# Performance work log

Hardware: AMD Instinct MI355X
Metric: run time of the kernel (lower is better)

Reference implementation:

```python
import jax, jax.numpy as jnp
import numpy as np

S, B, E2 = 128, 32, 1024   # src_len, batch, 2*encoder_hidden
DH = 512                   # decoder_hidden
AH = 32                    # attn_hidden
EMB = 256                  # embedding_dim
V = 32000                  # output_dim (vocab)


def setup_inputs() -> dict:
    key = jax.random.key(0)
    ks = jax.random.split(key, 14)
    sc = 0.02
    inp = {
        "encoder_output": jax.random.normal(ks[0], (S, B, E2), jnp.float32),
        "max_length": 48,
        "sos_token": 1,
        "emb": jax.random.normal(ks[1], (V, EMB), jnp.float32) * sc,
        "W1": jax.random.normal(ks[2], (AH, DH + E2), jnp.float32) * sc,
        "b1": jnp.zeros((AH,), jnp.float32),
        "W2": jax.random.normal(ks[3], (1, AH), jnp.float32) * sc,
        "b2": jnp.zeros((1,), jnp.float32),
        "W_ih": jax.random.normal(ks[4], (3 * DH, E2 + EMB), jnp.float32) * sc,
        "b_ih": jnp.zeros((3 * DH,), jnp.float32),
        "W_hh": jax.random.normal(ks[5], (3 * DH, DH), jnp.float32) * sc,
        "b_hh": jnp.zeros((3 * DH,), jnp.float32),
        "Wo": jax.random.normal(ks[6], (V, DH), jnp.float32) * sc,
        "bo": jnp.zeros((V,), jnp.float32),
    }
    return inp


def reference(encoder_output, max_length, sos_token, emb, W1, b1, W2, b2,
              W_ih, b_ih, W_hh, b_hh, Wo, bo):
    s, b, _ = encoder_output.shape
    dh = W_hh.shape[1]

    def step(carry, _):
        h, x_emb = carry                       # h: [B,DH], x_emb: [B,EMB]
        # Bahdanau-style attention: concat(hidden, enc) -> MLP -> softmax over S
        ai = jnp.concatenate(
            [jnp.broadcast_to(h[None], (s, b, dh)), encoder_output], axis=2)
        scores = jnp.maximum(ai @ W1.T + b1, 0.0) @ W2.T + b2   # [S,B,1]
        attn = jax.nn.softmax(scores[..., 0], axis=0)           # [S,B]
        context = jnp.einsum('sbe,sb->be', encoder_output, attn)  # [B,2E]
        # single-step GRU cell (torch gate order: r, z, n)
        x = jnp.concatenate([context, x_emb], axis=1)
        gi = x @ W_ih.T + b_ih
        gh = h @ W_hh.T + b_hh
        r = jax.nn.sigmoid(gi[:, :dh] + gh[:, :dh])
        z = jax.nn.sigmoid(gi[:, dh:2 * dh] + gh[:, dh:2 * dh])
        n = jnp.tanh(gi[:, 2 * dh:] + r * gh[:, 2 * dh:])
        h_new = (1.0 - z) * n + z * h
        logits = h_new @ Wo.T + bo                              # [B,V]
        ids = jnp.argmax(logits, axis=1)
        return (h_new, emb[ids]), logits

    h0 = jnp.zeros((b, dh), encoder_output.dtype)
    x0 = jnp.broadcast_to(emb[sos_token][None], (b, emb.shape[1]))
    _, out = jax.lax.scan(step, (h0, x0), None, length=max_length)
    return out  # [max_length, B, V]
```

## Files before the change

### kernel.cpp

```cpp
#include <hip/hip_runtime.h>
#include <hip/hip_bf16.h>
#include <math.h>

typedef __bf16 bf16x8 __attribute__((ext_vector_type(8)));
typedef __bf16 bf16x4 __attribute__((ext_vector_type(4)));
typedef float f32x4 __attribute__((ext_vector_type(4)));

#define S_LEN 128
#define BATCH 32
#define E2C 1024
#define DH 512
#define AH 32
#define EMBD 256
#define VOC 32000
#define TMAX 48
#define LCHN 250

#define MFMA16(a, b, c) __builtin_amdgcn_mfma_f32_16x16x32_bf16((a), (b), (c), 0, 0, 0)

#define OFF_HF0   0
#define OFF_HH0   65536
#define OFF_HL0   98304
#define OFF_HF1   131072
#define OFF_HH1   196608
#define OFF_HL1   229376
#define OFF_XH    262144
#define OFF_XL    344064
#define OFF_ENCW1 425984
#define OFF_PVAL  950272
#define OFF_PIDX  983040
#define OFF_WOH   1015808
#define OFF_WOL   33783808
#define OFF_WIHH  66551808
#define OFF_WIHL  70483968
#define OFF_WHHH  74416128
#define OFF_WHHL  75988992
#define WS_REQ    77561856ULL

__device__ __forceinline__ void split8(const float* __restrict__ p,
                                       bf16x8& hi, bf16x8& lo) {
  const f32x4 v0 = *(const f32x4*)p;
  const f32x4 v1 = *(const f32x4*)(p + 4);
  float t[8] = {v0[0], v0[1], v0[2], v0[3], v1[0], v1[1], v1[2], v1[3]};
  #pragma unroll
  for (int i = 0; i < 8; i++) {
    const __bf16 h = (__bf16)t[i];
    hi[i] = h;
    lo[i] = (__bf16)(t[i] - (float)h);
  }
}

__global__ __launch_bounds__(256) void k_init(unsigned int* __restrict__ p) {
  p[blockIdx.x * 256 + threadIdx.x] = 0u;
}

__global__ __launch_bounds__(256) void k_encw1(const float* __restrict__ enc,
                                               const float* __restrict__ W1,
                                               float* __restrict__ encW1) {
  __shared__ float el[E2C];
  __shared__ float red[256];
  const int tid = threadIdx.x;
  const int blk = blockIdx.x;
  for (int i = 0; i < 4; i++)
    el[tid + i * 256] = enc[(size_t)blk * E2C + tid + i * 256];
  __syncthreads();
  const int j = tid >> 3, c = tid & 7;
  const float* wrow = W1 + (size_t)j * (DH + E2C) + DH;
  float p = 0.f;
  for (int k = c * 128; k < c * 128 + 128; k++) p += el[k] * wrow[k];
  red[tid] = p;
  __syncthreads();
  if (c < 4) red[tid] += red[tid + 4];
  __syncthreads();
  if (c < 2) red[tid] += red[tid + 2];
  __syncthreads();
  if (c == 0) encW1[(size_t)blk * AH + j] = red[tid] + red[tid + 1];
}

__global__ __launch_bounds__(256) void k_split4(const float* __restrict__ src,
                                                __bf16* __restrict__ dh,
                                                __bf16* __restrict__ dl, int n4) {
  const int i = blockIdx.x * 256 + threadIdx.x;
  if (i >= n4) return;
  const f32x4 v = ((const f32x4*)src)[i];
  bf16x4 h4, l4;
  #pragma unroll
  for (int j = 0; j < 4; j++) {
    const float x = v[j];
    const __bf16 h = (__bf16)x;
    h4[j] = h;
    l4[j] = (__bf16)(x - (float)h);
  }
  *(bf16x4*)(dh + (size_t)i * 4) = h4;
  *(bf16x4*)(dl + (size_t)i * 4) = l4;
}

__global__ __launch_bounds__(256) void k_attn(int t,
    const float* __restrict__ enc, const int* __restrict__ sos,
    const float* __restrict__ emb,
    const float* __restrict__ W1, const float* __restrict__ b1,
    const float* __restrict__ W2, const float* __restrict__ b2,
    const float* __restrict__ encW1,
    const float* __restrict__ hf,
    const float* __restrict__ pval, const int* __restrict__ pidx,
    __bf16* __restrict__ xh, __bf16* __restrict__ xl) {
  __shared__ float hs[DH];
  __shared__ float hw[AH];
  __shared__ float sc[S_LEN];
  __shared__ float red[256];
  __shared__ int ri[256];
  __shared__ int s_id;
  const int tid = threadIdx.x;
  const int b = blockIdx.x >> 2;
  const int part = blockIdx.x & 3;

  if (part == 0) {
    if (t == 0) {
      if (tid == 0) s_id = sos[0];
    } else {
      if (tid < LCHN) { red[tid] = pval[b * 256 + tid]; ri[tid] = pidx[b * 256 + tid]; }
      else            { red[tid] = -INFINITY;           ri[tid] = 0x7fffffff; }
      __syncthreads();
      for (int off = 128; off >= 1; off >>= 1) {
        if (tid < off) {
          const float ov = red[tid + off]; const int oi = ri[tid + off];
          if (ov > red[tid] || (ov == red[tid] && oi < ri[tid])) { red[tid] = ov; ri[tid] = oi; }
        }
        __syncthreads();
      }
      if (tid == 0) s_id = ri[0];
    }
    __syncthreads();
    int id = s_id;
    if (id < 0 || id >= VOC) id = 0;
    const float e = emb[(size_t)id * EMBD + tid];
    const __bf16 eh = (__bf16)e;
    xh[b * 1280 + 1024 + tid] = eh;
    xl[b * 1280 + 1024 + tid] = (__bf16)(e - (float)eh);
  }

  hs[tid] = hf[b * DH + tid];
  hs[tid + 256] = hf[b * DH + tid + 256];
  __syncthreads();
  {
    const int j = tid >> 3, c = tid & 7;
    const float* wrow = W1 + (size_t)j * (DH + E2C);
    float p = 0.f;
    for (int k = c * 64; k < c * 64 + 64; k++) p += hs[k] * wrow[k];
    red[tid] = p;
  }
  __syncthreads();
  if ((tid & 7) < 4) red[tid] += red[tid + 4];
  __syncthreads();
  if ((tid & 7) < 2) red[tid] += red[tid + 2];
  __syncthreads();
  if ((tid & 7) == 0) hw[tid >> 3] = red[tid] + red[tid + 1] + b1[tid >> 3];
  __syncthreads();

  float ex = 0.f;
  if (tid < S_LEN) {
    const float* ew = encW1 + ((size_t)tid * BATCH + b) * AH;
    float sum = b2[0];
    #pragma unroll
    for (int j = 0; j < AH; j++) {
      const float v = ew[j] + hw[j];
      sum += fmaxf(v, 0.f) * W2[j];
    }
    sc[tid] = sum;
  }
  __syncthreads();
  if (tid < 128) red[tid] = sc[tid];
  __syncthreads();
  for (int off = 64; off >= 1; off >>= 1) {
    if (tid < off) red[tid] = fmaxf(red[tid], red[tid + off]);
    __syncthreads();
  }
  const float mx = red[0];
  __syncthreads();
  if (tid < 128) { ex = expf(sc[tid] - mx); red[tid] = ex; }
  __syncthreads();
  for (int off = 64; off >= 1; off >>= 1) {
    if (tid < off) red[tid] += red[tid + off];
    __syncthreads();
  }
  const float ssum = red[0];
  if (tid < 128) sc[tid] = ex / ssum;
  __syncthreads();

  const int e0 = part * 256 + tid;
  float aa = 0.f;
  for (int s = 0; s < S_LEN; s++)
    aa += sc[s] * enc[((size_t)s * BATCH + b) * E2C + e0];
  const __bf16 ch = (__bf16)aa;
  xh[b * 1280 + e0] = ch;
  xl[b * 1280 + e0] = (__bf16)(aa - (float)ch);
}

template<bool PRE>
__global__ __launch_bounds__(256) void k_gru(
    const __bf16* __restrict__ xh, const __bf16* __restrict__ xl,
    const float* __restrict__ Wih, const float* __restrict__ bih,
    const float* __restrict__ Whh, const float* __restrict__ bhh,
    const __bf16* __restrict__ Wihh, const __bf16* __restrict__ Wihl,
    const __bf16* __restrict__ Whhh, const __bf16* __restrict__ Whhl,
    const float* __restrict__ hf_in, const __bf16* __restrict__ hh_in,
    const __bf16* __restrict__ hl_in,
    float* __restrict__ hf_out, __bf16* __restrict__ hh_out,
    __bf16* __restrict__ hl_out) {
  __shared__ float lds[4][8][256];
  const int tid = threadIdx.x;
  const int wv = tid >> 6;
  const int lane = tid & 63;
  const int q = lane >> 4;
  const int ln = lane & 15;
  const int d = blockIdx.x * 16 + ln;

  f32x4 acc[4][2];
  const f32x4 z4 = {0.f, 0.f, 0.f, 0.f};
  #pragma unroll
  for (int t = 0; t < 4; t++) { acc[t][0] = z4; acc[t][1] = z4; }

  #pragma unroll
  for (int i = 0; i < 14; i++) {
    const int kk = wv * 32 + i * 128;
    const int ka = kk + q * 8;
    bf16x8 ah0, al0, ah1, al1;
    if (i < 10) {
      ah0 = *(const bf16x8*)(xh + ln * 1280 + ka);
      ah1 = *(const bf16x8*)(xh + (16 + ln) * 1280 + ka);
      al0 = *(const bf16x8*)(xl + ln * 1280 + ka);
      al1 = *(const bf16x8*)(xl + (16 + ln) * 1280 + ka);
    } else {
      const int kb = ka - 1280;
      ah0 = *(const bf16x8*)(hh_in + ln * 512 + kb);
      ah1 = *(const bf16x8*)(hh_in + (16 + ln) * 512 + kb);
      al0 = *(const bf16x8*)(hl_in + ln * 512 + kb);
      al1 = *(const bf16x8*)(hl_in + (16 + ln) * 512 + kb);
    }
    #pragma unroll
    for (int g = 0; g < 3; g++) {
      bf16x8 bh, bl;
      if (PRE) {
        if (i < 10) {
          bh = *(const bf16x8*)(Wihh + (size_t)(g * 512 + d) * 1280 + ka);
          bl = *(const bf16x8*)(Wihl + (size_t)(g * 512 + d) * 1280 + ka);
        } else {
          bh = *(const bf16x8*)(Whhh + (size_t)(g * 512 + d) * 512 + (ka - 1280));
          bl = *(const bf16x8*)(Whhl + (size_t)(g * 512 + d) * 512 + (ka - 1280));
        }
      } else {
        if (i < 10) split8(Wih + (size_t)(g * 512 + d) * 1280 + ka, bh, bl);
        else        split8(Whh + (size_t)(g * 512 + d) * 512 + (ka - 1280), bh, bl);
      }
      const int t = (g < 2) ? g : ((i < 10) ? 2 : 3);
      acc[t][0] = MFMA16(ah0, bh, acc[t][0]);
      acc[t][0] = MFMA16(al0, bh, acc[t][0]);
      acc[t][0] = MFMA16(ah0, bl, acc[t][0]);
      acc[t][1] = MFMA16(ah1, bh, acc[t][1]);
      acc[t][1] = MFMA16(al1, bh, acc[t][1]);
      acc[t][1] = MFMA16(ah1, bl, acc[t][1]);
    }
  }

  #pragma unroll
  for (int t = 0; t < 4; t++)
    #pragma unroll
    for (int mt = 0; mt < 2; mt++)
      #pragma unroll
      for (int r = 0; r < 4; r++)
        lds[wv][t * 2 + mt][(q * 4 + r) * 16 + ln] = acc[t][mt][r];
  __syncthreads();
  for (int idx = tid; idx < 8 * 256; idx += 256) {
    const int tt = idx >> 8, e = idx & 255;
    lds[0][tt][e] += lds[1][tt][e] + lds[2][tt][e] + lds[3][tt][e];
  }
  __syncthreads();

  for (int u = tid; u < 512; u += 256) {
    const int b = u >> 4, dd = u & 15;
    const int mt = b >> 4;
    const int e = (b & 15) * 16 + dd;
    const int dg = blockIdx.x * 16 + dd;
    const float rp  = lds[0][0 * 2 + mt][e] + bih[dg]        + bhh[dg];
    const float zp  = lds[0][1 * 2 + mt][e] + bih[DH + dg]   + bhh[DH + dg];
    const float gin = lds[0][2 * 2 + mt][e] + bih[2 * DH + dg];
    const float ghn = lds[0][3 * 2 + mt][e] + bhh[2 * DH + dg];
    const float rg = 1.f / (1.f + expf(-rp));
    const float zg = 1.f / (1.f + expf(-zp));
    const float ng = tanhf(gin + rg * ghn);
    const float hp = hf_in[b * DH + dg];
    const float hn = (1.f - zg) * ng + zg * hp;
    hf_out[b * DH + dg] = hn;
    const __bf16 hi = (__bf16)hn;
    hh_out[b * DH + dg] = hi;
    hl_out[b * DH + dg] = (__bf16)(hn - (float)hi);
  }
}

template<bool PRE>
__global__ __launch_bounds__(256) void k_logits(
    const __bf16* __restrict__ hh, const __bf16* __restrict__ hl,
    const float* __restrict__ Wo, const float* __restrict__ bo,
    const __bf16* __restrict__ Woh, const __bf16* __restrict__ Wol,
    float* __restrict__ outp, float* __restrict__ pval, int* __restrict__ pidx) {
  const int tid = threadIdx.x;
  const int w = tid >> 6;
  const int lane = tid & 63;
  const int quad = lane >> 4;
  const int ln = lane & 15;
  const int v0 = blockIdx.x * 128;

  f32x4 acc[2][2];
  const f32x4 z4 = {0.f, 0.f, 0.f, 0.f};
  #pragma unroll
  for (int m = 0; m < 2; m++)
    #pragma unroll
    for (int n = 0; n < 2; n++) acc[m][n] = z4;

  #pragma unroll 2
  for (int kk = 0; kk < 512; kk += 32) {
    const int ka = kk + quad * 8;
    const bf16x8 fh0 = *(const bf16x8*)(hh + ln * 512 + ka);
    const bf16x8 fh1 = *(const bf16x8*)(hh + (16 + ln) * 512 + ka);
    const bf16x8 fl0 = *(const bf16x8*)(hl + ln * 512 + ka);
    const bf16x8 fl1 = *(const bf16x8*)(hl + (16 + ln) * 512 + ka);
    #pragma unroll
    for (int nt = 0; nt < 2; nt++) {
      const int vr = v0 + (w * 2 + nt) * 16 + ln;
      bf16x8 bh, bl;
      if (PRE) {
        bh = *(const bf16x8*)(Woh + (size_t)vr * 512 + ka);
        bl = *(const bf16x8*)(Wol + (size_t)vr * 512 + ka);
      } else {
        split8(Wo + (size_t)vr * 512 + ka, bh, bl);
      }
      acc[0][nt] = MFMA16(fh0, bh, acc[0][nt]);
      acc[0][nt] = MFMA16(fl0, bh, acc[0][nt]);
      acc[0][nt] = MFMA16(fh0, bl, acc[0][nt]);
      acc[1][nt] = MFMA16(fh1, bh, acc[1][nt]);
      acc[1][nt] = MFMA16(fl1, bh, acc[1][nt]);
      acc[1][nt] = MFMA16(fh1, bl, acc[1][nt]);
    }
  }

  float bv[2][4]; int bi[2][4];
  #pragma unroll
  for (int m = 0; m < 2; m++)
    #pragma unroll
    for (int r = 0; r < 4; r++) { bv[m][r] = -INFINITY; bi[m][r] = 0x7fffffff; }

  #pragma unroll
  for (int nt = 0; nt < 2; nt++) {
    const int v = v0 + (w * 2 + nt) * 16 + ln;
    const float bias = bo[v];
    #pragma unroll
    for (int mt = 0; mt < 2; mt++) {
      #pragma unroll
      for (int r = 0; r < 4; r++) {
        const float val = acc[mt][nt][r] + bias;
        const int b = mt * 16 + quad * 4 + r;
        __builtin_nontemporal_store(val, &outp[(size_t)b * VOC + v]);
        if (val > bv[mt][r]) { bv[mt][r] = val; bi[mt][r] = v; }
      }
    }
  }
  #pragma unroll
  for (int m = 1; m < 16; m <<= 1) {
    #pragma unroll
    for (int mt = 0; mt < 2; mt++) {
      #pragma unroll
      for (int r = 0; r < 4; r++) {
        const float ov = __shfl_xor(bv[mt][r], m, 64);
        const int oi = __shfl_xor(bi[mt][r], m, 64);
        if (ov > bv[mt][r] || (ov == bv[mt][r] && oi < bi[mt][r])) {
          bv[mt][r] = ov; bi[mt][r] = oi;
        }
      }
    }
  }
  __shared__ float lv[128];
  __shared__ int li[128];
  if (ln == 0) {
    #pragma unroll
    for (int mt = 0; mt < 2; mt++)
      for (int r = 0; r < 4; r++) {
        const int b = mt * 16 + quad * 4 + r;
        lv[w * 32 + b] = bv[mt][r];
        li[w * 32 + b] = bi[mt][r];
      }
  }
  __syncthreads();
  if (tid < 32) {
    float bbv = lv[tid]; int bbi = li[tid];
    for (int w2 = 1; w2 < 4; w2++) {
      const float ov = lv[w2 * 32 + tid]; const int oi = li[w2 * 32 + tid];
      if (ov > bbv || (ov == bbv && oi < bbi)) { bbv = ov; bbi = oi; }
    }
    pval[tid * 256 + blockIdx.x] = bbv;
    pidx[tid * 256 + blockIdx.x] = bbi;
  }
}

extern "C" void kernel_launch(void* const* d_in, const int* in_sizes, int n_in,
                              void* d_out, int out_size, void* d_ws, size_t ws_size,
                              hipStream_t stream) {
  const float* enc = (const float*)d_in[0];
  const int* sos = (const int*)d_in[2];
  const float* emb = (const float*)d_in[3];
  const float* W1 = (const float*)d_in[4];
  const float* b1 = (const float*)d_in[5];
  const float* W2 = (const float*)d_in[6];
  const float* b2 = (const float*)d_in[7];
  const float* Wih = (const float*)d_in[8];
  const float* bih = (const float*)d_in[9];
  const float* Whh = (const float*)d_in[10];
  const float* bhh = (const float*)d_in[11];
  const float* Wo = (const float*)d_in[12];
  const float* bo = (const float*)d_in[13];

  char* ws = (char*)d_ws;
  float* hf[2]  = {(float*)(ws + OFF_HF0),  (float*)(ws + OFF_HF1)};
  __bf16* hh[2] = {(__bf16*)(ws + OFF_HH0), (__bf16*)(ws + OFF_HH1)};
  __bf16* hl[2] = {(__bf16*)(ws + OFF_HL0), (__bf16*)(ws + OFF_HL1)};
  __bf16* xh = (__bf16*)(ws + OFF_XH);
  __bf16* xl = (__bf16*)(ws + OFF_XL);
  float* encW1 = (float*)(ws + OFF_ENCW1);
  float* pval = (float*)(ws + OFF_PVAL);
  int* pidx = (int*)(ws + OFF_PIDX);
  __bf16* Woh  = (__bf16*)(ws + OFF_WOH);
  __bf16* Wol  = (__bf16*)(ws + OFF_WOL);
  __bf16* Wihh = (__bf16*)(ws + OFF_WIHH);
  __bf16* Wihl = (__bf16*)(ws + OFF_WIHL);
  __bf16* Whhh = (__bf16*)(ws + OFF_WHHH);
  __bf16* Whhl = (__bf16*)(ws + OFF_WHHL);

  k_init<<<128, 256, 0, stream>>>((unsigned int*)ws);
  k_encw1<<<S_LEN * BATCH, 256, 0, stream>>>(enc, W1, encW1);

  float* out = (float*)d_out;
  const bool pre = (ws_size >= WS_REQ);
  if (pre) {
    k_split4<<<16000, 256, 0, stream>>>(Wo,  Woh,  Wol,  4096000);
    k_split4<<<1920,  256, 0, stream>>>(Wih, Wihh, Wihl, 491520);
    k_split4<<<768,   256, 0, stream>>>(Whh, Whhh, Whhl, 196608);
  }

  for (int t = 0; t < TMAX; t++) {
    const int p = t & 1;
    k_attn<<<128, 256, 0, stream>>>(t, enc, sos, emb, W1, b1, W2, b2,
                                    encW1, hf[p], pval, pidx, xh, xl);
    if (pre) {
      k_gru<true><<<32, 256, 0, stream>>>(xh, xl, Wih, bih, Whh, bhh,
                                          Wihh, Wihl, Whhh, Whhl,
                                          hf[p], hh[p], hl[p],
                                          hf[p ^ 1], hh[p ^ 1], hl[p ^ 1]);
      k_logits<true><<<LCHN, 256, 0, stream>>>(hh[p ^ 1], hl[p ^ 1], Wo, bo, Woh, Wol,
                                               out + (size_t)t * BATCH * VOC, pval, pidx);
    } else {
      k_gru<false><<<32, 256, 0, stream>>>(xh, xl, Wih, bih, Whh, bhh,
                                           Wihh, Wihl, Whhh, Whhl,
                                           hf[p], hh[p], hl[p],
                                           hf[p ^ 1], hh[p ^ 1], hl[p ^ 1]);
      k_logits<false><<<LCHN, 256, 0, stream>>>(hh[p ^ 1], hl[p ^ 1], Wo, bo, Woh, Wol,
                                                out + (size_t)t * BATCH * VOC, pval, pidx);
    }
  }
}
```

Measured before the change: 3.079 ms.

## Fuse attention context into logits kernel and move argmax/embedding into GRU

Removes the per-step attention kernel. The context computation for the next step now runs as extra blocks appended to the logits launch, and a one-off context kernel covers step zero. The argmax reduction and embedding lookup move into the GRU kernel, which splits the embedding row to bf16 on the fly. The logits kernel goes to 512 threads with one 16-column tile per wave. The goal is one fewer launch and dependency point per decode step, at the cost of redundant argmax work in every GRU block.

Measured after the change: 3.341 ms. 8.5% more time.

```diff
diff --git a/kernel.cpp b/kernel.cpp
--- a/kernel.cpp
+++ b/kernel.cpp
@@ -15,6 +15,7 @@
 #define VOC 32000
 #define TMAX 48
 #define LCHN 250
+#define CTXB 64
 
 #define MFMA16(a, b, c) __builtin_amdgcn_mfma_f32_16x16x32_bf16((a), (b), (c), 0, 0, 0)
 
@@ -95,54 +96,22 @@
   *(bf16x4*)(dl + (size_t)i * 4) = l4;
 }
 
-__global__ __launch_bounds__(256) void k_attn(int t,
-    const float* __restrict__ enc, const int* __restrict__ sos,
-    const float* __restrict__ emb,
+__device__ __forceinline__ void ctx_block(int bc, int tid,
+    const float* __restrict__ enc,
     const float* __restrict__ W1, const float* __restrict__ b1,
     const float* __restrict__ W2, const float* __restrict__ b2,
-    const float* __restrict__ encW1,
-    const float* __restrict__ hf,
-    const float* __restrict__ pval, const int* __restrict__ pidx,
-    __bf16* __restrict__ xh, __bf16* __restrict__ xl) {
-  __shared__ float hs[DH];
-  __shared__ float hw[AH];
-  __shared__ float sc[S_LEN];
-  __shared__ float red[256];
-  __shared__ int ri[256];
-  __shared__ int s_id;
-  const int tid = threadIdx.x;
-  const int b = blockIdx.x >> 2;
-  const int part = blockIdx.x & 3;
-
-  if (part == 0) {
-    if (t == 0) {
-      if (tid == 0) s_id = sos[0];
-    } else {
-      if (tid < LCHN) { red[tid] = pval[b * 256 + tid]; ri[tid] = pidx[b * 256 + tid]; }
-      else            { red[tid] = -INFINITY;           ri[tid] = 0x7fffffff; }
-      __syncthreads();
-      for (int off = 128; off >= 1; off >>= 1) {
-        if (tid < off) {
-          const float ov = red[tid + off]; const int oi = ri[tid + off];
-          if (ov > red[tid] || (ov == red[tid] && oi < ri[tid])) { red[tid] = ov; ri[tid] = oi; }
-        }
-        __syncthreads();
-      }
-      if (tid == 0) s_id = ri[0];
-    }
-    __syncthreads();
-    int id = s_id;
-    if (id < 0 || id >= VOC) id = 0;
-    const float e = emb[(size_t)id * EMBD + tid];
-    const __bf16 eh = (__bf16)e;
-    xh[b * 1280 + 1024 + tid] = eh;
-    xl[b * 1280 + 1024 + tid] = (__bf16)(e - (float)eh);
-  }
-
-  hs[tid] = hf[b * DH + tid];
-  hs[tid + 256] = hf[b * DH + tid + 256];
-  __syncthreads();
-  {
+    const float* __restrict__ encW1, const float* __restrict__ hf,
+    __bf16* __restrict__ xh, __bf16* __restrict__ xl,
+    float* hs, float* hw, float* sc, float* red) {
+  const int b = bc >> 1;
+  const int part = bc & 1;
+
+  if (tid < 256) {
+    hs[tid] = hf[b * DH + tid];
+    hs[tid + 256] = hf[b * DH + tid + 256];
+  }
+  __syncthreads();
+  if (tid < 256) {
     const int j = tid >> 3, c = tid & 7;
     const float* wrow = W1 + (size_t)j * (DH + E2C);
     float p = 0.f;
@@ -150,11 +119,11 @@
     red[tid] = p;
   }
   __syncthreads();
-  if ((tid & 7) < 4) red[tid] += red[tid + 4];
-  __syncthreads();
-  if ((tid & 7) < 2) red[tid] += red[tid + 2];
-  __syncthreads();
-  if ((tid & 7) == 0) hw[tid >> 3] = red[tid] + red[tid + 1] + b1[tid >> 3];
+  if (tid < 256 && (tid & 7) < 4) red[tid] += red[tid + 4];
+  __syncthreads();
+  if (tid < 256 && (tid & 7) < 2) red[tid] += red[tid + 2];
+  __syncthreads();
+  if (tid < 256 && (tid & 7) == 0) hw[tid >> 3] = red[tid] + red[tid + 1] + b1[tid >> 3];
   __syncthreads();
 
   float ex = 0.f;
@@ -187,17 +156,33 @@
   if (tid < 128) sc[tid] = ex / ssum;
   __syncthreads();
 
-  const int e0 = part * 256 + tid;
+  const int e0 = part * 512 + tid;
   float aa = 0.f;
   for (int s = 0; s < S_LEN; s++)
     aa += sc[s] * enc[((size_t)s * BATCH + b) * E2C + e0];
   const __bf16 ch = (__bf16)aa;
-  xh[b * 1280 + e0] = ch;
-  xl[b * 1280 + e0] = (__bf16)(aa - (float)ch);
+  xh[b * 1024 + e0] = ch;
+  xl[b * 1024 + e0] = (__bf16)(aa - (float)ch);
+}
+
+__global__ __launch_bounds__(512) void k_ctx0(
+    const float* __restrict__ enc,
+    const float* __restrict__ W1, const float* __restrict__ b1,
+    const float* __restrict__ W2, const float* __restrict__ b2,
+    const float* __restrict__ encW1, const float* __restrict__ hf,
+    __bf16* __restrict__ xh, __bf16* __restrict__ xl) {
+  __shared__ float hs[DH];
+  __shared__ float hw[AH];
+  __shared__ float sc[S_LEN];
+  __shared__ float red[256];
+  ctx_block(blockIdx.x, threadIdx.x, enc, W1, b1, W2, b2, encW1, hf, xh, xl,
+            hs, hw, sc, red);
 }
 
 template<bool PRE>
-__global__ __launch_bounds__(256) void k_gru(
+__global__ __launch_bounds__(256) void k_gru(int t,
+    const int* __restrict__ sos, const float* __restrict__ emb,
+    const float* __restrict__ pval, const int* __restrict__ pidx,
     const __bf16* __restrict__ xh, const __bf16* __restrict__ xl,
     const float* __restrict__ Wih, const float* __restrict__ bih,
     const float* __restrict__ Whh, const float* __restrict__ bhh,
@@ -208,28 +193,67 @@
     float* __restrict__ hf_out, __bf16* __restrict__ hh_out,
     __bf16* __restrict__ hl_out) {
   __shared__ float lds[4][8][256];
+  __shared__ int ids[32];
   const int tid = threadIdx.x;
+
+  if (t == 0) {
+    if (tid < 32) {
+      int id = sos[0];
+      if (id < 0 || id >= VOC) id = 0;
+      ids[tid] = id;
+    }
+  } else {
+    float* sv = &lds[0][0][0];
+    int*   si = (int*)&lds[1][0][0];
+    const int b = tid >> 3, c0 = tid & 7;
+    float bv = -INFINITY; int bi = 0x7fffffff;
+    for (int c = c0; c < LCHN; c += 8) {
+      const float v = pval[b * 256 + c]; const int ix = pidx[b * 256 + c];
+      if (v > bv || (v == bv && ix < bi)) { bv = v; bi = ix; }
+    }
+    sv[tid] = bv; si[tid] = bi;
+    __syncthreads();
+    for (int off = 4; off >= 1; off >>= 1) {
+      if (c0 < off) {
+        const float ov = sv[tid + off]; const int oi = si[tid + off];
+        if (ov > sv[tid] || (ov == sv[tid] && oi < si[tid])) { sv[tid] = ov; si[tid] = oi; }
+      }
+      __syncthreads();
+    }
+    if (c0 == 0) {
+      int id = si[tid];
+      if (id < 0 || id >= VOC) id = 0;
+      ids[b] = id;
+    }
+  }
+  __syncthreads();
+
   const int wv = tid >> 6;
   const int lane = tid & 63;
   const int q = lane >> 4;
   const int ln = lane & 15;
   const int d = blockIdx.x * 16 + ln;
+  const int id0 = ids[ln];
+  const int id1 = ids[16 + ln];
 
   f32x4 acc[4][2];
   const f32x4 z4 = {0.f, 0.f, 0.f, 0.f};
   #pragma unroll
-  for (int t = 0; t < 4; t++) { acc[t][0] = z4; acc[t][1] = z4; }
+  for (int tt = 0; tt < 4; tt++) { acc[tt][0] = z4; acc[tt][1] = z4; }
 
   #pragma unroll
   for (int i = 0; i < 14; i++) {
-    const int kk = wv * 32 + i * 128;
-    const int ka = kk + q * 8;
+    const int ka = wv * 32 + i * 128 + q * 8;
     bf16x8 ah0, al0, ah1, al1;
-    if (i < 10) {
-      ah0 = *(const bf16x8*)(xh + ln * 1280 + ka);
-      ah1 = *(const bf16x8*)(xh + (16 + ln) * 1280 + ka);
-      al0 = *(const bf16x8*)(xl + ln * 1280 + ka);
-      al1 = *(const bf16x8*)(xl + (16 + ln) * 1280 + ka);
+    if (i < 8) {
+      ah0 = *(const bf16x8*)(xh + ln * 1024 + ka);
+      ah1 = *(const bf16x8*)(xh + (16 + ln) * 1024 + ka);
+      al0 = *(const bf16x8*)(xl + ln * 1024 + ka);
+      al1 = *(const bf16x8*)(xl + (16 + ln) * 1024 + ka);
+    } else if (i < 10) {
+      const int kb = ka - 1024;
+      split8(emb + (size_t)id0 * EMBD + kb, ah0, al0);
+      split8(emb + (size_t)id1 * EMBD + kb, ah1, al1);
     } else {
       const int kb = ka - 1280;
       ah0 = *(const bf16x8*)(hh_in + ln * 512 + kb);
@@ -252,23 +276,23 @@
         if (i < 10) split8(Wih + (size_t)(g * 512 + d) * 1280 + ka, bh, bl);
         else        split8(Whh + (size_t)(g * 512 + d) * 512 + (ka - 1280), bh, bl);
       }
-      const int t = (g < 2) ? g : ((i < 10) ? 2 : 3);
-      acc[t][0] = MFMA16(ah0, bh, acc[t][0]);
-      acc[t][0] = MFMA16(al0, bh, acc[t][0]);
-      acc[t][0] = MFMA16(ah0, bl, acc[t][0]);
-      acc[t][1] = MFMA16(ah1, bh, acc[t][1]);
-      acc[t][1] = MFMA16(al1, bh, acc[t][1]);
-      acc[t][1] = MFMA16(ah1, bl, acc[t][1]);
-    }
-  }
-
-  #pragma unroll
-  for (int t = 0; t < 4; t++)
+      const int tt = (g < 2) ? g : ((i < 10) ? 2 : 3);
+      acc[tt][0] = MFMA16(ah0, bh, acc[tt][0]);
+      acc[tt][0] = MFMA16(al0, bh, acc[tt][0]);
+      acc[tt][0] = MFMA16(ah0, bl, acc[tt][0]);
+      acc[tt][1] = MFMA16(ah1, bh, acc[tt][1]);
+      acc[tt][1] = MFMA16(al1, bh, acc[tt][1]);
+      acc[tt][1] = MFMA16(ah1, bl, acc[tt][1]);
+    }
+  }
+
+  #pragma unroll
+  for (int tt = 0; tt < 4; tt++)
     #pragma unroll
     for (int mt = 0; mt < 2; mt++)
       #pragma unroll
       for (int r = 0; r < 4; r++)
-        lds[wv][t * 2 + mt][(q * 4 + r) * 16 + ln] = acc[t][mt][r];
+        lds[wv][tt * 2 + mt][(q * 4 + r) * 16 + ln] = acc[tt][mt][r];
   __syncthreads();
   for (int idx = tid; idx < 8 * 256; idx += 256) {
     const int tt = idx >> 8, e = idx & 255;
@@ -298,24 +322,44 @@
 }
 
 template<bool PRE>
-__global__ __launch_bounds__(256) void k_logits(
-    const __bf16* __restrict__ hh, const __bf16* __restrict__ hl,
+__global__ __launch_bounds__(512) void k_logctx(
+    const float* __restrict__ enc,
+    const float* __restrict__ W1, const float* __restrict__ b1,
+    const float* __restrict__ W2, const float* __restrict__ b2,
+    const float* __restrict__ encW1,
     const float* __restrict__ Wo, const float* __restrict__ bo,
     const __bf16* __restrict__ Woh, const __bf16* __restrict__ Wol,
-    float* __restrict__ outp, float* __restrict__ pval, int* __restrict__ pidx) {
+    const float* __restrict__ hf, const __bf16* __restrict__ hh,
+    const __bf16* __restrict__ hl,
+    float* __restrict__ outp, float* __restrict__ pval, int* __restrict__ pidx,
+    __bf16* __restrict__ xh, __bf16* __restrict__ xl) {
+  __shared__ union {
+    struct { float hs[DH]; float hw[AH]; float sc[S_LEN]; float red[256]; } c;
+    struct { float lv[256]; int li[256]; } l;
+  } sm;
   const int tid = threadIdx.x;
+  const int blk = blockIdx.x;
+
+  if (blk >= LCHN) {
+    ctx_block(blk - LCHN, tid, enc, W1, b1, W2, b2, encW1, hf, xh, xl,
+              sm.c.hs, sm.c.hw, sm.c.sc, sm.c.red);
+    return;
+  }
+
   const int w = tid >> 6;
   const int lane = tid & 63;
   const int quad = lane >> 4;
   const int ln = lane & 15;
-  const int v0 = blockIdx.x * 128;
-
-  f32x4 acc[2][2];
+  const int v0 = blk * 128;
+  const int vr = v0 + w * 16 + ln;
+
+  f32x4 acc[2];
   const f32x4 z4 = {0.f, 0.f, 0.f, 0.f};
-  #pragma unroll
-  for (int m = 0; m < 2; m++)
-    #pragma unroll
-    for (int n = 0; n < 2; n++) acc[m][n] = z4;
+  acc[0] = z4; acc[1] = z4;
+
+  const __bf16* wrh = Woh + (size_t)vr * 512;
+  const __bf16* wrl = Wol + (size_t)vr * 512;
+  const float*  wrf = Wo  + (size_t)vr * 512;
 
   #pragma unroll 2
   for (int kk = 0; kk < 512; kk += 32) {
@@ -324,44 +368,31 @@
     const bf16x8 fh1 = *(const bf16x8*)(hh + (16 + ln) * 512 + ka);
     const bf16x8 fl0 = *(const bf16x8*)(hl + ln * 512 + ka);
     const bf16x8 fl1 = *(const bf16x8*)(hl + (16 + ln) * 512 + ka);
+    bf16x8 bh, bl;
+    if (PRE) {
+      bh = *(const bf16x8*)(wrh + ka);
+      bl = *(const bf16x8*)(wrl + ka);
+    } else {
+      split8(wrf + ka, bh, bl);
+    }
+    acc[0] = MFMA16(fh0, bh, acc[0]);
+    acc[0] = MFMA16(fl0, bh, acc[0]);
+    acc[0] = MFMA16(fh0, bl, acc[0]);
+    acc[1] = MFMA16(fh1, bh, acc[1]);
+    acc[1] = MFMA16(fl1, bh, acc[1]);
+    acc[1] = MFMA16(fh1, bl, acc[1]);
+  }
+
+  float bv[2][4]; int bi[2][4];
+  const float bias = bo[vr];
+  #pragma unroll
+  for (int mt = 0; mt < 2; mt++) {
     #pragma unroll
-    for (int nt = 0; nt < 2; nt++) {
-      const int vr = v0 + (w * 2 + nt) * 16 + ln;
-      bf16x8 bh, bl;
-      if (PRE) {
-        bh = *(const bf16x8*)(Woh + (size_t)vr * 512 + ka);
-        bl = *(const bf16x8*)(Wol + (size_t)vr * 512 + ka);
-      } else {
-        split8(Wo + (size_t)vr * 512 + ka, bh, bl);
-      }
-      acc[0][nt] = MFMA16(fh0, bh, acc[0][nt]);
-      acc[0][nt] = MFMA16(fl0, bh, acc[0][nt]);
-      acc[0][nt] = MFMA16(fh0, bl, acc[0][nt]);
-      acc[1][nt] = MFMA16(fh1, bh, acc[1][nt]);
-      acc[1][nt] = MFMA16(fl1, bh, acc[1][nt]);
-      acc[1][nt] = MFMA16(fh1, bl, acc[1][nt]);
-    }
-  }
-
-  float bv[2][4]; int bi[2][4];
-  #pragma unroll
-  for (int m = 0; m < 2; m++)
-    #pragma unroll
-    for (int r = 0; r < 4; r++) { bv[m][r] = -INFINITY; bi[m][r] = 0x7fffffff; }
-
-  #pragma unroll
-  for (int nt = 0; nt < 2; nt++) {
-    const int v = v0 + (w * 2 + nt) * 16 + ln;
-    const float bias = bo[v];
-    #pragma unroll
-    for (int mt = 0; mt < 2; mt++) {
-      #pragma unroll
-      for (int r = 0; r < 4; r++) {
-        const float val = acc[mt][nt][r] + bias;
-        const int b = mt * 16 + quad * 4 + r;
-        __builtin_nontemporal_store(val, &outp[(size_t)b * VOC + v]);
-        if (val > bv[mt][r]) { bv[mt][r] = val; bi[mt][r] = v; }
-      }
+    for (int r = 0; r < 4; r++) {
+      const float val = acc[mt][r] + bias;
+      const int b = mt * 16 + quad * 4 + r;
+      __builtin_nontemporal_store(val, &outp[(size_t)b * VOC + vr]);
+      bv[mt][r] = val; bi[mt][r] = vr;
     }
   }
   #pragma unroll
@@ -378,26 +409,24 @@
       }
     }
   }
-  __shared__ float lv[128];
-  __shared__ int li[128];
   if (ln == 0) {
     #pragma unroll
     for (int mt = 0; mt < 2; mt++)
       for (int r = 0; r < 4; r++) {
         const int b = mt * 16 + quad * 4 + r;
-        lv[w * 32 + b] = bv[mt][r];
-        li[w * 32 + b] = bi[mt][r];
+        sm.l.lv[w * 32 + b] = bv[mt][r];
+        sm.l.li[w * 32 + b] = bi[mt][r];
       }
   }
   __syncthreads();
   if (tid < 32) {
-    float bbv = lv[tid]; int bbi = li[tid];
-    for (int w2 = 1; w2 < 4; w2++) {
-      const float ov = lv[w2 * 32 + tid]; const int oi = li[w2 * 32 + tid];
+    float bbv = sm.l.lv[tid]; int bbi = sm.l.li[tid];
+    for (int w2 = 1; w2 < 8; w2++) {
+      const float ov = sm.l.lv[w2 * 32 + tid]; const int oi = sm.l.li[w2 * 32 + tid];
       if (ov > bbv || (ov == bbv && oi < bbi)) { bbv = ov; bbi = oi; }
     }
-    pval[tid * 256 + blockIdx.x] = bbv;
-    pidx[tid * 256 + blockIdx.x] = bbi;
+    pval[tid * 256 + blk] = bbv;
+    pidx[tid * 256 + blk] = bbi;
   }
 }
 
@@ -444,25 +473,32 @@
     k_split4<<<1920,  256, 0, stream>>>(Wih, Wihh, Wihl, 491520);
     k_split4<<<768,   256, 0, stream>>>(Whh, Whhh, Whhl, 196608);
   }
+  k_ctx0<<<CTXB, 512, 0, stream>>>(enc, W1, b1, W2, b2, encW1, hf[0], xh, xl);
 
   for (int t = 0; t < TMAX; t++) {
     const int p = t & 1;
-    k_attn<<<128, 256, 0, stream>>>(t, enc, sos, emb, W1, b1, W2, b2,
-                                    encW1, hf[p], pval, pidx, xh, xl);
     if (pre) {
-      k_gru<true><<<32, 256, 0, stream>>>(xh, xl, Wih, bih, Whh, bhh,
+      k_gru<true><<<32, 256, 0, stream>>>(t, sos, emb, pval, pidx, xh, xl,
+                                          Wih, bih, Whh, bhh,
                                           Wihh, Wihl, Whhh, Whhl,
                                           hf[p], hh[p], hl[p],
                                           hf[p ^ 1], hh[p ^ 1], hl[p ^ 1]);
-      k_logits<true><<<LCHN, 256, 0, stream>>>(hh[p ^ 1], hl[p ^ 1], Wo, bo, Woh, Wol,
-                                               out + (size_t)t * BATCH * VOC, pval, pidx);
+      k_logctx<true><<<LCHN + CTXB, 512, 0, stream>>>(enc, W1, b1, W2, b2, encW1,
+                                          Wo, bo, Woh, Wol,
+                                          hf[p ^ 1], hh[p ^ 1], hl[p ^ 1],
+                                          out + (size_t)t * BATCH * VOC,
+                                          pval, pidx, xh, xl);
     } else {
-      k_gru<false><<<32, 256, 0, stream>>>(xh, xl, Wih, bih, Whh, bhh,
-                                           Wihh, Wihl, Whhh, Whhl,
-                                           hf[p], hh[p], hl[p],
-                                           hf[p ^ 1], hh[p ^ 1], hl[p ^ 1]);
-      k_logits<false><<<LCHN, 256, 0, stream>>>(hh[p ^ 1], hl[p ^ 1], Wo, bo, Woh, Wol,
-                                                out + (size_t)t * BATCH * VOC, pval, pidx);
-    }
-  }
-}
+      k_gru<false><<<32, 256, 0, stream>>>(t, sos, emb, pval, pidx, xh, xl,
+                                          Wih, bih, Whh, bhh,
+                                          Wihh, Wihl, Whhh, Whhl,
+                                          hf[p], hh[p], hl[p],
+                                          hf[p ^ 1], hh[p ^ 1], hl[p ^ 1]);
+      k_logctx<false><<<LCHN + CTXB, 512, 0, stream>>>(enc, W1, b1, W2, b2, encW1,
+                                          Wo, bo, Woh, Wol,
+                                          hf[p ^ 1], hh[p ^ 1], hl[p ^ 1],
+                                          out + (size_t)t * BATCH * VOC,
+                                          pval, pidx, xh, xl);
+    }
+  }
+}
```
